# Kernel optimization log

Hardware: AMD Instinct MI355X
Metric: run time of the kernel (lower is better)

The kernel has to match this reference:

```python
import jax, jax.numpy as jnp
import numpy as np

BLOCK = 8
ITERS = 8
EPS = 1e-5
SHAPE = (64, 64, 64)
BATCH = 16


def overlapping_blocks(x, bs):
    # x: [B, M, N, K] -> per-block copies with a 1-cell zero-padded halo:
    # [B, nm, nn, nk, bs+2, bs+2, bs+2]
    B, M, N, K = x.shape
    p = jnp.pad(x, ((0, 0), (1, 1), (1, 1), (1, 1)))

    def gather(a, axis, n, size):
        idx = (jnp.arange(n)[:, None] * bs + jnp.arange(size)[None, :]).reshape(-1)
        a = jnp.take(a, idx, axis=axis)
        return a.reshape(a.shape[:axis] + (n, size) + a.shape[axis + 1:])

    nm, nn, nk = M // bs, N // bs, K // bs
    p = gather(p, 1, nm, bs + 2)   # [B, nm, P, N+2, K+2]
    p = gather(p, 3, nn, bs + 2)   # [B, nm, P, nn, P, K+2]
    p = gather(p, 5, nk, bs + 2)   # [B, nm, P, nn, P, nk, P]
    return p.transpose(0, 1, 3, 5, 2, 4, 6)


def param_blocks(w, bs):
    # [..., M, N, K] -> [..., nm, nn, nk, bs, bs, bs] (non-overlapping)
    lead = w.shape[:-3]
    M, N, K = w.shape[-3:]
    w = w.reshape(*lead, M // bs, bs, N // bs, bs, K // bs, bs)
    nl = len(lead)
    perm = tuple(range(nl)) + (nl, nl + 2, nl + 4, nl + 1, nl + 3, nl + 5)
    return w.transpose(perm)


def gridnet_step(weight, bias, residual_scale, x, inner_iterations, block_size,
                 eps=EPS, normalize=True):
    bs = block_size
    blocks = overlapping_blocks(x, bs)            # [B, nm, nn, nk, P, P, P]
    wb = param_blocks(weight, bs)                 # [27, nm, nn, nk, bs, bs, bs]
    bb = param_blocks(bias, bs)                   # [nm, nn, nk, bs, bs, bs]
    rb = param_blocks(residual_scale, bs)
    inner = (slice(None),) * 4 + (slice(1, -1),) * 3

    for _ in range(inner_iterations):
        if normalize:
            mean = blocks.mean(axis=(-3, -2, -1), keepdims=True)
            var = blocks.var(axis=(-3, -2, -1), keepdims=True)
            normed = (blocks - mean) / jnp.sqrt(var + eps)
        else:
            normed = blocks
        dot = jnp.zeros_like(blocks[inner])
        tap = 0
        for dx in range(3):
            for dy in range(3):
                for dz in range(3):
                    nb = normed[..., dx:dx + bs, dy:dy + bs, dz:dz + bs]
                    dot = dot + nb * wb[tap]
                    tap += 1
        out = blocks[inner] + rb * jax.nn.silu(dot + bb)
        # only interior cells update; halo stays at initial (synced) values
        blocks = blocks.at[inner].set(out)

    y = blocks[inner]                              # [B, nm, nn, nk, bs, bs, bs]
    B, nm, nn, nk = y.shape[:4]
    return y.transpose(0, 1, 4, 2, 5, 3, 6).reshape(B, nm * bs, nn * bs, nk * bs)


def setup_inputs() -> dict:
    key = jax.random.key(0)
    k_w, k_x = jax.random.split(key)
    M, N, K = SHAPE
    weight = jax.random.normal(k_w, (27, M, N, K), dtype=jnp.float32) / np.sqrt(27.0).astype(np.float32)
    bias = jnp.zeros((M, N, K), dtype=jnp.float32)
    residual_scale = jnp.ones((M, N, K), dtype=jnp.float32)
    x = jax.random.normal(k_x, (BATCH, M, N, K), dtype=jnp.float32)
    return {"weight": weight, "bias": bias, "residual_scale": residual_scale, "x": x}


def reference(weight, bias, residual_scale, x):
    return gridnet_step(weight, bias, residual_scale, x, ITERS, BLOCK, EPS, True)
```

## Files before the change

### kernel.cpp

```cpp
#include <hip/hip_runtime.h>

typedef _Float16 h2 __attribute__((ext_vector_type(2)));

#define COLH 10

template <int CTRL>
__device__ __forceinline__ float dpp_stage(float v) {
    int x = __builtin_amdgcn_update_dpp(0, __float_as_int(v), CTRL, 0xf, 0xf, true);
    return v + __int_as_float(x);
}
__device__ __forceinline__ float wave_sum(float v) {
    v = dpp_stage<0x111>(v);
    v = dpp_stage<0x112>(v);
    v = dpp_stage<0x114>(v);
    v = dpp_stage<0x118>(v);
    v = dpp_stage<0x142>(v);
    v = dpp_stage<0x143>(v);
    return v;
}

#define RFL(x) __int_as_float(__builtin_amdgcn_readfirstlane(__float_as_int(x)))

__device__ __forceinline__ h2 mid2(h2 lo, h2 hi) {
    int r = __builtin_amdgcn_alignbit(__builtin_bit_cast(int, hi),
                                      __builtin_bit_cast(int, lo), 16);
    return __builtin_bit_cast(h2, r);
}

#define R27(M) M(0) M(1) M(2) M(3) M(4) M(5) M(6) M(7) M(8) M(9) M(10) M(11) \
    M(12) M(13) M(14) M(15) M(16) M(17) M(18) M(19) M(20) M(21) M(22) M(23)  \
    M(24) M(25) M(26)
#define R9L(M) M(0) M(1) M(2) M(3) M(4) M(5) M(6) M(7) M(8)

#define LOADW(T) float2 f##T = *(const float2*)(W + ((size_t)(T) << 18) + ofs); \
                 h2 w##T = { (_Float16)f##T.x, (_Float16)f##T.y };              \
                 sw0 += (float)w##T.x; sw1 += (float)w##T.y;

#define LINE(L, WA, WB, WC) {                                                 \
    const h2 v0 = bp[(((L) / 3) * 10 + (L) % 3) * 5];                         \
    const h2 v1 = bp[(((L) / 3) * 10 + (L) % 3) * 5 + 1];                     \
    const h2 vm = mid2(v0, v1);                                               \
    dd = __builtin_elementwise_fma(v0, WA, dd);                               \
    dd = __builtin_elementwise_fma(vm, WB, dd);                               \
    dd = __builtin_elementwise_fma(v1, WC, dd);  }

#define ITER(SRC, DST, RED) {                                                 \
    const h2* bp = (const h2*)&SRC[base_h];                                   \
    float mean = (halo_s + Si) * inv_n;                                       \
    float istd = rsqrtf((halo_q + Qi) * inv_n - mean * mean + 1e-5f);         \
    h2 dd = { (_Float16)0.f, (_Float16)0.f };                                 \
    LINE(0, w0,  w1,  w2)                                                     \
    LINE(1, w3,  w4,  w5)                                                     \
    LINE(2, w6,  w7,  w8)                                                     \
    LINE(3, w9,  w10, w11)                                                    \
    LINE(4, w12, w13, w14)                                                    \
    LINE(5, w15, w16, w17)                                                    \
    LINE(6, w18, w19, w20)                                                    \
    LINE(7, w21, w22, w23)                                                    \
    LINE(8, w24, w25, w26)                                                    \
    float u0 = ((float)dd.x - mean * sw0) * istd + bias0;                     \
    float u1 = ((float)dd.y - mean * sw1) * istd + bias1;                     \
    c0 += rs0 * (u0 * __builtin_amdgcn_rcpf(1.f + __expf(-u0)));              \
    c1 += rs1 * (u1 * __builtin_amdgcn_rcpf(1.f + __expf(-u1)));              \
    DST[ipc]     = (_Float16)c0;                                              \
    DST[ipc + 1] = (_Float16)c1;                                              \
    float b0 = wave_sum(c0 + c1);                                             \
    float b1 = wave_sum(c0 * c0 + c1 * c1);                                   \
    if (lane == 63) RED[wave] = make_float2(b0, b1);                          \
    __syncthreads();                                                          \
    Si = RFL(RED[0].x + RED[1].x + RED[2].x + RED[3].x);                      \
    Qi = RFL(RED[0].y + RED[1].y + RED[2].y + RED[3].y); }

__global__ __launch_bounds__(256)
void gridnet_kernel(const float* __restrict__ W,
                    const float* __restrict__ Bias,
                    const float* __restrict__ Rs,
                    const float* __restrict__ X,
                    float* __restrict__ Y,
                    int n_batch)
{
    __shared__ __align__(16) _Float16 buf0[100 * COLH];
    __shared__ __align__(16) _Float16 buf1[100 * COLH];
    __shared__ float4 red4[4];
    __shared__ float2 redA[4], redB[4];

    const int tid  = threadIdx.x;
    const int h    = tid & 3;
    const int ly   = (tid >> 2) & 7;
    const int lx   = tid >> 5;
    const int wave = tid >> 6;
    const int lane = tid & 63;

    const int bid   = blockIdx.x;
    const int r     = bid / n_batch;
    const int batch = bid - r * n_batch;
    const int gm0 = (r >> 6) << 3;
    const int gn0 = ((r >> 3) & 7) << 3;
    const int gk0 = (r & 7) << 3;

    const float* xb = X + ((size_t)batch << 18);

    float s_all = 0.f, q_all = 0.f, s_int = 0.f, q_int = 0.f;
    for (int i = tid; i < 1000; i += 256) {
        int ix = i / 100;
        int rem = i - ix * 100;
        int iy = rem / 10;
        int iz = rem - iy * 10;
        int m = gm0 + ix - 1, n = gn0 + iy - 1, k = gk0 + iz - 1;
        float v = 0.f;
        if ((unsigned)m < 64u && (unsigned)n < 64u && (unsigned)k < 64u)
            v = xb[(m << 12) + (n << 6) + k];
        _Float16 hv = (_Float16)v;
        int a = (ix * 10 + iy) * COLH + iz;
        buf0[a] = hv;
        buf1[a] = hv;
        float vf = (float)hv;
        s_all += vf;
        q_all += vf * vf;
        bool interior = ((unsigned)(ix - 1) < 8u) & ((unsigned)(iy - 1) < 8u) &
                        ((unsigned)(iz - 1) < 8u);
        if (interior) { s_int += vf; q_int += vf * vf; }
    }

    const int gm = gm0 + lx, gn = gn0 + ly, gk = gk0 + 2 * h;
    const size_t ofs = ((size_t)gm << 12) + (gn << 6) + gk;

    float sw0 = 0.f, sw1 = 0.f;
    R27(LOADW)
    const float2 bf = *(const float2*)(Bias + ofs);
    const float2 rf = *(const float2*)(Rs + ofs);
    const float bias0 = bf.x, bias1 = bf.y;
    const float rs0 = rf.x, rs1 = rf.y;

    __syncthreads();

    const int base_h = (lx * 10 + ly) * COLH + 2 * h;
    const int ipc    = ((lx + 1) * 10 + (ly + 1)) * COLH + (2 * h + 1);
    float c0 = (float)buf0[ipc];
    float c1 = (float)buf0[ipc + 1];

    float a0 = wave_sum(s_all);
    float a1 = wave_sum(q_all);
    float a2 = wave_sum(s_int);
    float a3 = wave_sum(q_int);
    if (lane == 63) red4[wave] = make_float4(a0, a1, a2, a3);
    __syncthreads();
    float S_all = 0.f, Q_all = 0.f, Si = 0.f, Qi = 0.f;
    #pragma unroll
    for (int wv = 0; wv < 4; ++wv) {
        float4 t4 = red4[wv];
        S_all += t4.x; Q_all += t4.y; Si += t4.z; Qi += t4.w;
    }
    const float halo_s = RFL(S_all - Si);
    const float halo_q = RFL(Q_all - Qi);
    Si = RFL(Si);
    Qi = RFL(Qi);

    const float inv_n = 1.0f / 1000.0f;

    #pragma unroll 1
    for (int it = 0; it < 4; ++it) {
        ITER(buf0, buf1, redA)
        ITER(buf1, buf0, redB)
    }

    *(float2*)(Y + ((size_t)batch << 18) + ofs) = make_float2(c0, c1);
}

extern "C" void kernel_launch(void* const* d_in, const int* in_sizes, int n_in,
                              void* d_out, int out_size, void* d_ws, size_t ws_size,
                              hipStream_t stream) {
    const float* W = (const float*)d_in[0];
    const float* B = (const float*)d_in[1];
    const float* R = (const float*)d_in[2];
    const float* X = (const float*)d_in[3];
    float* Y = (float*)d_out;

    int n_batch = in_sizes[3] >> 18;
    dim3 grid(512 * n_batch), block(256);
    hipLaunchKernelGGL(gridnet_kernel, grid, block, 0, stream, W, B, R, X, Y, n_batch);
}
```

Before: 166.4 us.

## Compute four outputs per thread with 128-thread blocks and widened LDS rows

Each thread now computes four consecutive z-outputs using two packed-half accumulators instead of two, so the block shrinks to 128 threads (two waves). LDS rows are padded to 12 halves with a one-element offset so each thread reads aligned 8-byte chunks and reuses the loaded values across both pairs. The normalisation affine step and bias are also done in packed half precision. The intent is fewer LDS loads per output, wider global loads, and a cheaper cross-wave reduction. The cost is more registers per thread, fewer waves for latency hiding, and extra fp16 rounding in the normalisation.

```diff
diff --git a/kernel.cpp b/kernel.cpp
--- a/kernel.cpp
+++ b/kernel.cpp
@@ -2,7 +2,7 @@
 
 typedef _Float16 h2 __attribute__((ext_vector_type(2)));
 
-#define COLH 10
+#define COLH 12
 
 template <int CTRL>
 __device__ __forceinline__ float dpp_stage(float v) {
@@ -30,48 +30,70 @@
 #define R27(M) M(0) M(1) M(2) M(3) M(4) M(5) M(6) M(7) M(8) M(9) M(10) M(11) \
     M(12) M(13) M(14) M(15) M(16) M(17) M(18) M(19) M(20) M(21) M(22) M(23)  \
     M(24) M(25) M(26)
-#define R9L(M) M(0) M(1) M(2) M(3) M(4) M(5) M(6) M(7) M(8)
-
-#define LOADW(T) float2 f##T = *(const float2*)(W + ((size_t)(T) << 18) + ofs); \
-                 h2 w##T = { (_Float16)f##T.x, (_Float16)f##T.y };              \
-                 sw0 += (float)w##T.x; sw1 += (float)w##T.y;
-
-#define LINE(L, WA, WB, WC) {                                                 \
-    const h2 v0 = bp[(((L) / 3) * 10 + (L) % 3) * 5];                         \
-    const h2 v1 = bp[(((L) / 3) * 10 + (L) % 3) * 5 + 1];                     \
-    const h2 vm = mid2(v0, v1);                                               \
-    dd = __builtin_elementwise_fma(v0, WA, dd);                               \
-    dd = __builtin_elementwise_fma(vm, WB, dd);                               \
-    dd = __builtin_elementwise_fma(v1, WC, dd);  }
-
-#define ITER(SRC, DST, RED) {                                                 \
-    const h2* bp = (const h2*)&SRC[base_h];                                   \
+
+#define DECLW(T) h2 wa##T, wb##T;
+#define LOADW(T) { float4 f = *(const float4*)(W + ((size_t)(T) << 18) + ofs);  \
+    wa##T.x = (_Float16)f.x; wa##T.y = (_Float16)f.y;                           \
+    wb##T.x = (_Float16)f.z; wb##T.y = (_Float16)f.w;                           \
+    s0 += (float)wa##T.x; s1 += (float)wa##T.y;                                 \
+    s2 += (float)wb##T.x; s3 += (float)wb##T.y; }
+
+#define LINE(CD, T0, T1, T2) {                                                \
+    const uint2 q0 = qp[(CD) * 3];                                            \
+    const uint2 q1 = qp[(CD) * 3 + 1];                                        \
+    const h2 d0 = __builtin_bit_cast(h2, q0.x);                               \
+    const h2 d1 = __builtin_bit_cast(h2, q0.y);                               \
+    const h2 d2 = __builtin_bit_cast(h2, q1.x);                               \
+    const h2 d3 = __builtin_bit_cast(h2, q1.y);                               \
+    const h2 a1 = mid2(d0, d1);                                               \
+    const h2 a3 = mid2(d1, d2);                                               \
+    const h2 a5 = mid2(d2, d3);                                               \
+    ddA = __builtin_elementwise_fma(a1, wa##T0, ddA);                         \
+    ddA = __builtin_elementwise_fma(d1, wa##T1, ddA);                         \
+    ddA = __builtin_elementwise_fma(a3, wa##T2, ddA);                         \
+    ddB = __builtin_elementwise_fma(a3, wb##T0, ddB);                         \
+    ddB = __builtin_elementwise_fma(d2, wb##T1, ddB);                         \
+    ddB = __builtin_elementwise_fma(a5, wb##T2, ddB); }
+
+#define ITER(QP, WP, RED) {                                                   \
+    const uint2* qp = QP;                                                     \
     float mean = (halo_s + Si) * inv_n;                                       \
     float istd = rsqrtf((halo_q + Qi) * inv_n - mean * mean + 1e-5f);         \
-    h2 dd = { (_Float16)0.f, (_Float16)0.f };                                 \
-    LINE(0, w0,  w1,  w2)                                                     \
-    LINE(1, w3,  w4,  w5)                                                     \
-    LINE(2, w6,  w7,  w8)                                                     \
-    LINE(3, w9,  w10, w11)                                                    \
-    LINE(4, w12, w13, w14)                                                    \
-    LINE(5, w15, w16, w17)                                                    \
-    LINE(6, w18, w19, w20)                                                    \
-    LINE(7, w21, w22, w23)                                                    \
-    LINE(8, w24, w25, w26)                                                    \
-    float u0 = ((float)dd.x - mean * sw0) * istd + bias0;                     \
-    float u1 = ((float)dd.y - mean * sw1) * istd + bias1;                     \
+    h2 mneg; mneg.x = (_Float16)(-mean); mneg.y = mneg.x;                     \
+    h2 isth; isth.x = (_Float16)istd;    isth.y = isth.x;                     \
+    h2 ddA = {(_Float16)0.f, (_Float16)0.f};                                  \
+    h2 ddB = ddA;                                                             \
+    LINE(0,   0,  1,  2)                                                      \
+    LINE(1,   3,  4,  5)                                                      \
+    LINE(2,   6,  7,  8)                                                      \
+    LINE(10,  9, 10, 11)                                                      \
+    LINE(11, 12, 13, 14)                                                      \
+    LINE(12, 15, 16, 17)                                                      \
+    LINE(20, 18, 19, 20)                                                      \
+    LINE(21, 21, 22, 23)                                                      \
+    LINE(22, 24, 25, 26)                                                      \
+    h2 uA = __builtin_elementwise_fma(swA, mneg, ddA);                        \
+    h2 uB = __builtin_elementwise_fma(swB, mneg, ddB);                        \
+    uA = __builtin_elementwise_fma(uA, isth, bA);                             \
+    uB = __builtin_elementwise_fma(uB, isth, bB);                             \
+    float u0 = (float)uA.x, u1 = (float)uA.y;                                 \
+    float u2 = (float)uB.x, u3 = (float)uB.y;                                 \
     c0 += rs0 * (u0 * __builtin_amdgcn_rcpf(1.f + __expf(-u0)));              \
     c1 += rs1 * (u1 * __builtin_amdgcn_rcpf(1.f + __expf(-u1)));              \
-    DST[ipc]     = (_Float16)c0;                                              \
-    DST[ipc + 1] = (_Float16)c1;                                              \
-    float b0 = wave_sum(c0 + c1);                                             \
-    float b1 = wave_sum(c0 * c0 + c1 * c1);                                   \
+    c2 += rs2 * (u2 * __builtin_amdgcn_rcpf(1.f + __expf(-u2)));              \
+    c3 += rs3 * (u3 * __builtin_amdgcn_rcpf(1.f + __expf(-u3)));              \
+    h2 cp0; cp0.x = (_Float16)c0; cp0.y = (_Float16)c1;                       \
+    h2 cp1; cp1.x = (_Float16)c2; cp1.y = (_Float16)c3;                       \
+    (WP)[0] = cp0;                                                            \
+    (WP)[1] = cp1;                                                            \
+    float b0 = wave_sum(c0 + c1 + c2 + c3);                                   \
+    float b1 = wave_sum(c0 * c0 + c1 * c1 + c2 * c2 + c3 * c3);               \
     if (lane == 63) RED[wave] = make_float2(b0, b1);                          \
     __syncthreads();                                                          \
-    Si = RFL(RED[0].x + RED[1].x + RED[2].x + RED[3].x);                      \
-    Qi = RFL(RED[0].y + RED[1].y + RED[2].y + RED[3].y); }
-
-__global__ __launch_bounds__(256)
+    Si = RFL(RED[0].x + RED[1].x);                                            \
+    Qi = RFL(RED[0].y + RED[1].y); }
+
+__global__ __launch_bounds__(128)
 void gridnet_kernel(const float* __restrict__ W,
                     const float* __restrict__ Bias,
                     const float* __restrict__ Rs,
@@ -81,13 +103,13 @@
 {
     __shared__ __align__(16) _Float16 buf0[100 * COLH];
     __shared__ __align__(16) _Float16 buf1[100 * COLH];
-    __shared__ float4 red4[4];
-    __shared__ float2 redA[4], redB[4];
+    __shared__ float4 red4[2];
+    __shared__ float2 redA[2], redB[2];
 
     const int tid  = threadIdx.x;
-    const int h    = tid & 3;
-    const int ly   = (tid >> 2) & 7;
-    const int lx   = tid >> 5;
+    const int h    = tid & 1;
+    const int y    = (tid >> 1) & 7;
+    const int x    = tid >> 4;
     const int wave = tid >> 6;
     const int lane = tid & 63;
 
@@ -101,7 +123,7 @@
     const float* xb = X + ((size_t)batch << 18);
 
     float s_all = 0.f, q_all = 0.f, s_int = 0.f, q_int = 0.f;
-    for (int i = tid; i < 1000; i += 256) {
+    for (int i = tid; i < 1000; i += 128) {
         int ix = i / 100;
         int rem = i - ix * 100;
         int iy = rem / 10;
@@ -111,7 +133,7 @@
         if ((unsigned)m < 64u && (unsigned)n < 64u && (unsigned)k < 64u)
             v = xb[(m << 12) + (n << 6) + k];
         _Float16 hv = (_Float16)v;
-        int a = (ix * 10 + iy) * COLH + iz;
+        int a = (ix * 10 + iy) * COLH + 1 + iz;
         buf0[a] = hv;
         buf1[a] = hv;
         float vf = (float)hv;
@@ -122,22 +144,31 @@
         if (interior) { s_int += vf; q_int += vf * vf; }
     }
 
-    const int gm = gm0 + lx, gn = gn0 + ly, gk = gk0 + 2 * h;
-    const size_t ofs = ((size_t)gm << 12) + (gn << 6) + gk;
-
-    float sw0 = 0.f, sw1 = 0.f;
+    const int gm = gm0 + x, gn = gn0 + y;
+    const size_t ofs = ((size_t)gm << 12) + (gn << 6) + gk0 + 4 * h;
+
+    R27(DECLW)
+    float s0 = 0.f, s1 = 0.f, s2 = 0.f, s3 = 0.f;
     R27(LOADW)
-    const float2 bf = *(const float2*)(Bias + ofs);
-    const float2 rf = *(const float2*)(Rs + ofs);
-    const float bias0 = bf.x, bias1 = bf.y;
-    const float rs0 = rf.x, rs1 = rf.y;
+    h2 swA; swA.x = (_Float16)s0; swA.y = (_Float16)s1;
+    h2 swB; swB.x = (_Float16)s2; swB.y = (_Float16)s3;
+    const float4 bf = *(const float4*)(Bias + ofs);
+    const float4 rf = *(const float4*)(Rs + ofs);
+    h2 bA; bA.x = (_Float16)bf.x; bA.y = (_Float16)bf.y;
+    h2 bB; bB.x = (_Float16)bf.z; bB.y = (_Float16)bf.w;
+    const float rs0 = rf.x, rs1 = rf.y, rs2 = rf.z, rs3 = rf.w;
 
     __syncthreads();
 
-    const int base_h = (lx * 10 + ly) * COLH + 2 * h;
-    const int ipc    = ((lx + 1) * 10 + (ly + 1)) * COLH + (2 * h + 1);
-    float c0 = (float)buf0[ipc];
-    float c1 = (float)buf0[ipc + 1];
+    const uint2* qp0 = (const uint2*)(buf0 + (x * 10 + y) * COLH + 4 * h);
+    const uint2* qp1 = (const uint2*)(buf1 + (x * 10 + y) * COLH + 4 * h);
+    const int widx = ((x + 1) * 10 + (y + 1)) * COLH + 2 + 4 * h;
+    h2* wp0 = (h2*)(buf0 + widx);
+    h2* wp1 = (h2*)(buf1 + widx);
+
+    h2 ci0 = wp0[0], ci1 = wp0[1];
+    float c0 = (float)ci0.x, c1 = (float)ci0.y;
+    float c2 = (float)ci1.x, c3 = (float)ci1.y;
 
     float a0 = wave_sum(s_all);
     float a1 = wave_sum(q_all);
@@ -145,26 +176,21 @@
     float a3 = wave_sum(q_int);
     if (lane == 63) red4[wave] = make_float4(a0, a1, a2, a3);
     __syncthreads();
-    float S_all = 0.f, Q_all = 0.f, Si = 0.f, Qi = 0.f;
-    #pragma unroll
-    for (int wv = 0; wv < 4; ++wv) {
-        float4 t4 = red4[wv];
-        S_all += t4.x; Q_all += t4.y; Si += t4.z; Qi += t4.w;
-    }
-    const float halo_s = RFL(S_all - Si);
-    const float halo_q = RFL(Q_all - Qi);
-    Si = RFL(Si);
-    Qi = RFL(Qi);
+    float4 t0 = red4[0], t1 = red4[1];
+    const float halo_s = RFL((t0.x + t1.x) - (t0.z + t1.z));
+    const float halo_q = RFL((t0.y + t1.y) - (t0.w + t1.w));
+    float Si = RFL(t0.z + t1.z);
+    float Qi = RFL(t0.w + t1.w);
 
     const float inv_n = 1.0f / 1000.0f;
 
     #pragma unroll 1
     for (int it = 0; it < 4; ++it) {
-        ITER(buf0, buf1, redA)
-        ITER(buf1, buf0, redB)
+        ITER(qp0, wp1, redA)
+        ITER(qp1, wp0, redB)
     }
 
-    *(float2*)(Y + ((size_t)batch << 18) + ofs) = make_float2(c0, c1);
+    *(float4*)(Y + ((size_t)batch << 18) + ofs) = make_float4(c0, c1, c2, c3);
 }
 
 extern "C" void kernel_launch(void* const* d_in, const int* in_sizes, int n_in,
@@ -177,6 +203,6 @@
     float* Y = (float*)d_out;
 
     int n_batch = in_sizes[3] >> 18;
-    dim3 grid(512 * n_batch), block(256);
+    dim3 grid(512 * n_batch), block(128);
     hipLaunchKernelGGL(gridnet_kernel, grid, block, 0, stream, W, B, R, X, Y, n_batch);
 }
```

Result: slower. 175.4 us (+5.4%).
